# Optimization experiments

Measured on AMD Instinct MI355X. Metric: run time of the kernel, lower is better.

## Reference

```python
import jax, jax.numpy as jnp
import numpy as np

B, T, D = 64, 1024, 512
H, O = 512, 128
HALF = D // 2
ALPHA_M = 0.8


def setup_inputs() -> dict:
    key = jax.random.key(0)
    ks = jax.random.split(key, 6)
    s_in = 1.0 / np.sqrt(HALF)
    s_h = 1.0 / np.sqrt(H)
    return {
        "x": jax.random.normal(ks[0], (B, T, D), dtype=jnp.float32),
        "w1": jax.random.uniform(ks[1], (H, HALF), jnp.float32, -s_in, s_in),
        "b1": jnp.zeros((H,), jnp.float32),
        "tau1": jnp.full((H,), 3.0, jnp.float32),
        "w2": jax.random.uniform(ks[2], (H, HALF), jnp.float32, -s_in, s_in),
        "b2": jnp.zeros((H,), jnp.float32),
        "tau2": jnp.full((H,), 0.5, jnp.float32),
        "wo": jax.random.uniform(ks[3], (O, H), jnp.float32, -s_h, s_h),
        "bo": jnp.zeros((O,), jnp.float32),
    }


def reference(x, w1, b1, tau1, w2, b2, tau2, wo, bo):
    # Hoist the per-timestep branch Linears into two batched GEMMs.
    d1_in = jnp.einsum("bti,hi->tbh", x[:, :, :HALF], w1) + b1  # [T,B,H]
    d2_in = jnp.einsum("bti,hi->tbh", x[:, :, HALF:], w2) + b2  # [T,B,H]

    a1 = jax.nn.sigmoid(tau1)  # [H]
    a2 = jax.nn.sigmoid(tau2)  # [H]

    def step(carry, ins):
        d1, d2, mem = carry
        i1, i2 = ins
        d1 = a1 * d1 + (1.0 - a1) * i1
        d2 = a2 * d2 + (1.0 - a2) * i2
        mem = ALPHA_M * mem + (1.0 - ALPHA_M) * (d1 + d2)
        return (d1, d2, mem), mem

    z = jnp.zeros((x.shape[0], tau1.shape[0]), x.dtype)
    _, mems = jax.lax.scan(step, (z, z, z), (d1_in, d2_in))  # mems: [T,B,H]

    # Output projection + sigmoid, vectorized over all timesteps.
    out = jax.nn.sigmoid(jnp.einsum("tbh,oh->bto", mems, wo) + bo)  # [B,T,O]
    return out
```

## Files before the change

### kernel.cpp

```cpp
#include <hip/hip_runtime.h>


#define B_    64
#define T_    1024
#define D_    512
#define H_    512
#define O_    128
#define HALF_ 256
#define CLEN  32
#define NC    32

typedef __attribute__((ext_vector_type(4))) float        f32x4;
typedef __attribute__((ext_vector_type(2))) float        f32x2;
typedef __attribute__((ext_vector_type(8))) short        s16x8;
typedef __attribute__((ext_vector_type(4))) unsigned int u32x4;
typedef __attribute__((ext_vector_type(2))) unsigned int u32x2;

__device__ __forceinline__ unsigned short f2bf(float f) {
    unsigned u = __float_as_uint(f);
    return (unsigned short)((u + 0x7fffu + ((u >> 16) & 1u)) >> 16);
}
__device__ __forceinline__ unsigned packbf(float a, float b) {
    return (unsigned)f2bf(a) | ((unsigned)f2bf(b) << 16);
}
__device__ __forceinline__ float bflo(unsigned u) { return __uint_as_float(u << 16); }
__device__ __forceinline__ float bfhi(unsigned u) { return __uint_as_float(u & 0xffff0000u); }
__device__ __forceinline__ float sigf(float x) { return 1.f / (1.f + __expf(-x)); }
__device__ __forceinline__ float guard(float dn) {
    if (fabsf(dn) < 1e-6f) dn = (dn < 0.f ? -1e-6f : 1e-6f);
    return dn;
}
__device__ __forceinline__ float pw32(float a) {
    float t = a * a; t *= t; t *= t; t *= t; t *= t; return t;
}

typedef const __attribute__((address_space(1))) unsigned int gu32;
typedef __attribute__((address_space(3))) unsigned int      lu32;
__device__ __forceinline__ void gl_lds16(const void* g, void* l) {
    __builtin_amdgcn_global_load_lds((gu32*)g, (lu32*)l, 16, 0, 0);
}

__global__ __launch_bounds__(256) void gtab_kernel(
    const float* __restrict__ tau1, const float* __restrict__ tau2,
    float* __restrict__ G1, float* __restrict__ G2)
{
    const int h = blockIdx.x * 256 + threadIdx.x;
    const float a1 = sigf(tau1[h]), a2 = sigf(tau2[h]);
    const float c1 = 0.2f * a1 / guard(0.8f - a1);
    const float c2 = 0.2f * a2 / guard(0.8f - a2);
    float pm = 1.f, p1 = 1.f, p2 = 1.f;
    for (int k = 0; k < CLEN; ++k) {
        pm *= 0.8f; p1 *= a1; p2 *= a2;
        G1[k * H_ + h] = c1 * (pm - p1);
        G2[k * H_ + h] = c2 * (pm - p2);
    }
}

__global__ __launch_bounds__(256) void wcast_kernel(
    const float* __restrict__ w1, const float* __restrict__ w2,
    const float* __restrict__ wo,
    unsigned int* __restrict__ w1b, unsigned int* __restrict__ w2b,
    unsigned int* __restrict__ wob)
{
    const float* s; unsigned int* d; int n;
    if (blockIdx.y == 0)      { s = w1; d = w1b; n = H_ * HALF_; }
    else if (blockIdx.y == 1) { s = w2; d = w2b; n = H_ * HALF_; }
    else                      { s = wo; d = wob; n = O_ * H_;    }
    int i = (blockIdx.x * 256 + threadIdx.x) * 4;
    if (i >= n) return;
    f32x4 a = *(const f32x4*)(s + i);
    u32x2 p;
    p.x = packbf(a.x, a.y);
    p.y = packbf(a.z, a.w);
    *(u32x2*)(d + i / 2) = p;
}

__global__ __launch_bounds__(256) void cast_kernel(const float* __restrict__ x,
                                                   unsigned int* __restrict__ xb) {
    size_t i = ((size_t)blockIdx.x * 256 + threadIdx.x) * 8;
    f32x4 a = *(const f32x4*)(x + i);
    f32x4 b = *(const f32x4*)(x + i + 4);
    u32x4 p;
    p.x = packbf(a.x, a.y); p.y = packbf(a.z, a.w);
    p.z = packbf(b.x, b.y); p.w = packbf(b.z, b.w);
    *(u32x4*)(xb + i / 2) = p;
}

__global__ __launch_bounds__(256, 2) void gemm1f_kernel(
    const unsigned short* __restrict__ xb,
    const unsigned short* __restrict__ w1b, const unsigned short* __restrict__ w2b,
    const float* __restrict__ b1, const float* __restrict__ tau1,
    const float* __restrict__ b2, const float* __restrict__ tau2,
    unsigned int* __restrict__ mems,
    float* __restrict__ Sd1, float* __restrict__ Sd2, float* __restrict__ Sm)
{
    __shared__ short smem[32768];
    short* As1 = smem;
    short* As2 = smem + 8192;
    short* Bs1 = smem + 16384;
    short* Bs2 = smem + 24576;
    short* d1L = smem;
    short* d2L = smem + 16384;

    const int nt = blockIdx.x;
    const int mt = blockIdx.y;
    const int b  = mt >> 3;
    const int t0 = (mt & 7) << 7;

    const int tid = threadIdx.x, l = tid & 63, wv = tid >> 6;
    const int ln = l & 15, qd = l >> 4;
    const int wm = (wv & 1) << 6, wn = (wv >> 1) << 6;

    const unsigned short* abase  = xb + (size_t)(mt * 128) * D_;
    const unsigned short* w1base = w1b + (size_t)(nt * 128) * HALF_;
    const unsigned short* w2base = w2b + (size_t)(nt * 128) * HALF_;

    f32x4 acc0[4][4] = {};
    f32x4 acc1[4][4] = {};

    for (int kt = 0; kt < HALF_; kt += 64) {
        #pragma unroll
        for (int i = 0; i < 4; ++i) {
            int ch = wv * 4 + i;
            int r  = ch * 8 + (l >> 3);
            int kbl = (l & 7) ^ (r & 7);
            gl_lds16(abase + (size_t)r * D_ + kt + kbl * 8,         &As1[ch * 512 + l * 8]);
        }
        #pragma unroll
        for (int i = 0; i < 4; ++i) {
            int ch = wv * 4 + i;
            int r  = ch * 8 + (l >> 3);
            int kbl = (l & 7) ^ (r & 7);
            gl_lds16(abase + (size_t)r * D_ + HALF_ + kt + kbl * 8, &As2[ch * 512 + l * 8]);
        }
        #pragma unroll
        for (int i = 0; i < 4; ++i) {
            int ch = wv * 4 + i;
            int r  = ch * 8 + (l >> 3);
            int kbl = (l & 7) ^ (r & 7);
            gl_lds16(w1base + (size_t)r * HALF_ + kt + kbl * 8,     &Bs1[ch * 512 + l * 8]);
        }
        #pragma unroll
        for (int i = 0; i < 4; ++i) {
            int ch = wv * 4 + i;
            int r  = ch * 8 + (l >> 3);
            int kbl = (l & 7) ^ (r & 7);
            gl_lds16(w2base + (size_t)r * HALF_ + kt + kbl * 8,     &Bs2[ch * 512 + l * 8]);
        }
        __syncthreads();
        #pragma unroll
        for (int ks = 0; ks < 64; ks += 32) {
            s16x8 af[4], bfv[4];
            #pragma unroll
            for (int i = 0; i < 4; ++i) {
                int r = wm + i * 16 + ln;
                int kbp = ((ks >> 3) + qd) ^ (r & 7);
                af[i] = *(const s16x8*)&As1[r * 64 + kbp * 8];
            }
            #pragma unroll
            for (int j = 0; j < 4; ++j) {
                int r = wn + j * 16 + ln;
                int kbp = ((ks >> 3) + qd) ^ (r & 7);
                bfv[j] = *(const s16x8*)&Bs1[r * 64 + kbp * 8];
            }
            #pragma unroll
            for (int i = 0; i < 4; ++i)
                #pragma unroll
                for (int j = 0; j < 4; ++j)
                    acc0[i][j] = __builtin_amdgcn_mfma_f32_16x16x32_bf16(
                        af[i], bfv[j], acc0[i][j], 0, 0, 0);
            #pragma unroll
            for (int i = 0; i < 4; ++i) {
                int r = wm + i * 16 + ln;
                int kbp = ((ks >> 3) + qd) ^ (r & 7);
                af[i] = *(const s16x8*)&As2[r * 64 + kbp * 8];
            }
            #pragma unroll
            for (int j = 0; j < 4; ++j) {
                int r = wn + j * 16 + ln;
                int kbp = ((ks >> 3) + qd) ^ (r & 7);
                bfv[j] = *(const s16x8*)&Bs2[r * 64 + kbp * 8];
            }
            #pragma unroll
            for (int i = 0; i < 4; ++i)
                #pragma unroll
                for (int j = 0; j < 4; ++j)
                    acc1[i][j] = __builtin_amdgcn_mfma_f32_16x16x32_bf16(
                        af[i], bfv[j], acc1[i][j], 0, 0, 0);
        }
        __syncthreads();
    }

    #pragma unroll
    for (int i = 0; i < 4; ++i)
        #pragma unroll
        for (int j = 0; j < 4; ++j)
            #pragma unroll
            for (int r = 0; r < 4; ++r) {
                int t  = wm + i * 16 + qd * 4 + r;
                int hc = (wn + j * 16 + ln) ^ ((t & 12) << 2);
                d1L[t * 128 + hc] = (short)f2bf(acc0[i][j][r]);
                d2L[t * 128 + hc] = (short)f2bf(acc1[i][j][r]);
            }
    __syncthreads();

    const int cl  = tid >> 6;
    const int h2l = tid & 63;
    const int hl0 = h2l << 1;
    const int hg0 = nt * 128 + hl0;
    const int cg  = ((mt & 7) << 2) + cl;

    const float a1a = sigf(tau1[hg0]), a1b = sigf(tau1[hg0 + 1]);
    const float a2a = sigf(tau2[hg0]), a2b = sigf(tau2[hg0 + 1]);
    const float o1a = 1.f - a1a, o1b = 1.f - a1b;
    const float o2a = 1.f - a2a, o2b = 1.f - a2b;
    const float bb1a = b1[hg0], bb1b = b1[hg0 + 1];
    const float bb2a = b2[hg0], bb2b = b2[hg0 + 1];

    float d1a = 0.f, d1b = 0.f, d2a = 0.f, d2b = 0.f, ma = 0.f, mb = 0.f;
    const size_t mrow = (size_t)(b * T_ + t0 + cl * CLEN) * (H_ / 2) + nt * 64 + h2l;

    #pragma unroll 8
    for (int k = 0; k < CLEN; ++k) {
        int t  = cl * CLEN + k;
        int hc = hl0 ^ ((t & 12) << 2);
        unsigned u1 = *(const unsigned*)&d1L[t * 128 + hc];
        unsigned u2 = *(const unsigned*)&d2L[t * 128 + hc];
        float i1a = bflo(u1) + bb1a, i1b = bfhi(u1) + bb1b;
        float i2a = bflo(u2) + bb2a, i2b = bfhi(u2) + bb2b;
        d1a = a1a * d1a + o1a * i1a;  d1b = a1b * d1b + o1b * i1b;
        d2a = a2a * d2a + o2a * i2a;  d2b = a2b * d2b + o2b * i2b;
        ma = 0.8f * ma + 0.2f * (d1a + d2a);
        mb = 0.8f * mb + 0.2f * (d1b + d2b);
        mems[mrow + (size_t)k * (H_ / 2)] = packbf(ma, mb);
    }

    const size_t si = (size_t)(cg * B_ + b) * H_ + hg0;
    f32x2 v;
    v.x = d1a; v.y = d1b; *(f32x2*)&Sd1[si] = v;
    v.x = d2a; v.y = d2b; *(f32x2*)&Sd2[si] = v;
    v.x = ma;  v.y = mb;  *(f32x2*)&Sm[si]  = v;
}

__global__ __launch_bounds__(128) void scanB_kernel(
    const float* __restrict__ Sd1, const float* __restrict__ Sd2,
    const float* __restrict__ Sm,
    const float* __restrict__ tau1, const float* __restrict__ tau2,
    float* __restrict__ D1, float* __restrict__ D2, float* __restrict__ DM)
{
    const int g = blockIdx.x * 128 + threadIdx.x;
    const int h2 = g & 255, b = g >> 8, h0 = h2 << 1;

    const float a1a = sigf(tau1[h0]), a1b = sigf(tau1[h0 + 1]);
    const float a2a = sigf(tau2[h0]), a2b = sigf(tau2[h0 + 1]);
    const float amL = pw32(0.8f);
    const float a1La = pw32(a1a), a1Lb = pw32(a1b);
    const float a2La = pw32(a2a), a2Lb = pw32(a2b);

    const float c1a = 0.2f * a1a / guard(0.8f - a1a);
    const float c1b = 0.2f * a1b / guard(0.8f - a1b);
    const float c2a = 0.2f * a2a / guard(0.8f - a2a);
    const float c2b = 0.2f * a2b / guard(0.8f - a2b);

    const float g1La = c1a * (amL - a1La), g1Lb = c1b * (amL - a1Lb);
    const float g2La = c2a * (amL - a2La), g2Lb = c2b * (amL - a2Lb);

    float D1a = 0.f, D1b = 0.f, D2a = 0.f, D2b = 0.f, Ma = 0.f, Mb = 0.f;
    for (int c = 0; c < NC; ++c) {
        const size_t si = (size_t)(c * B_ + b) * H_ + h0;
        f32x2 v;
        v.x = D1a; v.y = D1b; *(f32x2*)&D1[si] = v;
        v.x = D2a; v.y = D2b; *(f32x2*)&D2[si] = v;
        v.x = Ma;  v.y = Mb;  *(f32x2*)&DM[si] = v;
        f32x2 s1 = *(const f32x2*)&Sd1[si];
        f32x2 s2 = *(const f32x2*)&Sd2[si];
        f32x2 sm = *(const f32x2*)&Sm[si];
        float nMa = amL * Ma + D1a * g1La + D2a * g2La + sm.x;
        float nMb = amL * Mb + D1b * g1Lb + D2b * g2Lb + sm.y;
        D1a = a1La * D1a + s1.x;  D1b = a1Lb * D1b + s1.y;
        D2a = a2La * D2a + s2.x;  D2b = a2Lb * D2b + s2.y;
        Ma = nMa;  Mb = nMb;
    }
}

__global__ __launch_bounds__(256, 2) void gemm2f_kernel(
    const unsigned short* __restrict__ mems, const unsigned short* __restrict__ wob,
    const float* __restrict__ bo,
    const float* __restrict__ G1, const float* __restrict__ G2,
    const float* __restrict__ D1, const float* __restrict__ D2,
    const float* __restrict__ DM, float* __restrict__ out)
{
    __shared__ short As[128 * 64];
    __shared__ short Bs[128 * 64];
    __shared__ float PMl[CLEN];

    const int mt = blockIdx.x;
    const int b = mt >> 3, c0 = (mt & 7) << 2;
    const int tid = threadIdx.x, l = tid & 63, wv = tid >> 6;
    const int ln = l & 15, qd = l >> 4;
    const int wm = (wv & 1) << 6, wn = (wv >> 1) << 6;

    if (tid < CLEN) {
        float pm = 1.f;
        for (int k = 0; k <= tid; ++k) pm *= 0.8f;
        PMl[tid] = pm;
    }
    __syncthreads();

    f32x4 acc[4][4] = {};
    const unsigned short* abase = mems + (size_t)(mt * 128) * H_;

    for (int kt = 0; kt < H_; kt += 64) {
        #pragma unroll
        for (int i = 0; i < 4; ++i) {
            int ch = wv * 4 + i;
            int r  = ch * 8 + (l >> 3);
            int kbl = (l & 7) ^ (r & 7);
            gl_lds16(wob + (size_t)r * H_ + kt + kbl * 8, &Bs[ch * 512 + l * 8]);
        }
        #pragma unroll
        for (int i = 0; i < 4; ++i) {
            int gi = i * 256 + tid;
            int r = gi >> 3, kbp = gi & 7, kbl = kbp ^ (r & 7);
            int h0 = kt + kbl * 8;
            int k = r & 31, c = c0 + (r >> 5);
            size_t dbase = (size_t)(c * B_ + b) * H_ + h0;
            f32x4 d1a = *(const f32x4*)&D1[dbase], d1b = *(const f32x4*)&D1[dbase + 4];
            f32x4 d2a = *(const f32x4*)&D2[dbase], d2b = *(const f32x4*)&D2[dbase + 4];
            f32x4 dma = *(const f32x4*)&DM[dbase], dmb = *(const f32x4*)&DM[dbase + 4];
            f32x4 g1a = *(const f32x4*)&G1[k * H_ + h0], g1b = *(const f32x4*)&G1[k * H_ + h0 + 4];
            f32x4 g2a = *(const f32x4*)&G2[k * H_ + h0], g2b = *(const f32x4*)&G2[k * H_ + h0 + 4];
            float pm = PMl[k];
            u32x4 mv = *(const u32x4*)(abase + (size_t)r * H_ + h0);
            float v0 = bflo(mv.x) + d1a.x * g1a.x + d2a.x * g2a.x + dma.x * pm;
            float v1 = bfhi(mv.x) + d1a.y * g1a.y + d2a.y * g2a.y + dma.y * pm;
            float v2 = bflo(mv.y) + d1a.z * g1a.z + d2a.z * g2a.z + dma.z * pm;
            float v3 = bfhi(mv.y) + d1a.w * g1a.w + d2a.w * g2a.w + dma.w * pm;
            float v4 = bflo(mv.z) + d1b.x * g1b.x + d2b.x * g2b.x + dmb.x * pm;
            float v5 = bfhi(mv.z) + d1b.y * g1b.y + d2b.y * g2b.y + dmb.y * pm;
            float v6 = bflo(mv.w) + d1b.z * g1b.z + d2b.z * g2b.z + dmb.z * pm;
            float v7 = bfhi(mv.w) + d1b.w * g1b.w + d2b.w * g2b.w + dmb.w * pm;
            u32x4 p;
            p.x = packbf(v0, v1); p.y = packbf(v2, v3);
            p.z = packbf(v4, v5); p.w = packbf(v6, v7);
            *(u32x4*)&As[r * 64 + kbp * 8] = p;
        }
        __syncthreads();
        #pragma unroll
        for (int ks = 0; ks < 64; ks += 32) {
            s16x8 af[4], bfv[4];
            #pragma unroll
            for (int i = 0; i < 4; ++i) {
                int r = wm + i * 16 + ln;
                int kbp = ((ks >> 3) + qd) ^ (r & 7);
                af[i] = *(const s16x8*)&As[r * 64 + kbp * 8];
            }
            #pragma unroll
            for (int j = 0; j < 4; ++j) {
                int r = wn + j * 16 + ln;
                int kbp = ((ks >> 3) + qd) ^ (r & 7);
                bfv[j] = *(const s16x8*)&Bs[r * 64 + kbp * 8];
            }
            #pragma unroll
            for (int i = 0; i < 4; ++i)
                #pragma unroll
                for (int j = 0; j < 4; ++j)
                    acc[i][j] = __builtin_amdgcn_mfma_f32_16x16x32_bf16(
                        af[i], bfv[j], acc[i][j], 0, 0, 0);
        }
        __syncthreads();
    }

    float bov[4];
    #pragma unroll
    for (int j = 0; j < 4; ++j) bov[j] = bo[wn + j * 16 + ln];

    float* orow = out + (size_t)(mt * 128 + wm + qd * 4) * O_ + wn + ln;
    #pragma unroll
    for (int i = 0; i < 4; ++i)
        #pragma unroll
        for (int j = 0; j < 4; ++j)
            #pragma unroll
            for (int r = 0; r < 4; ++r) {
                float v = acc[i][j][r] + bov[j];
                orow[(size_t)(i * 16 + r) * O_ + j * 16] = 1.f / (1.f + __expf(-v));
            }
}

extern "C" void kernel_launch(void* const* d_in, const int* in_sizes, int n_in,
                              void* d_out, int out_size, void* d_ws, size_t ws_size,
                              hipStream_t stream) {
    const float* x    = (const float*)d_in[0];
    const float* w1   = (const float*)d_in[1];
    const float* b1   = (const float*)d_in[2];
    const float* tau1 = (const float*)d_in[3];
    const float* w2   = (const float*)d_in[4];
    const float* b2   = (const float*)d_in[5];
    const float* tau2 = (const float*)d_in[6];
    const float* wo   = (const float*)d_in[7];
    const float* bo   = (const float*)d_in[8];
    float* out = (float*)d_out;

    char* w = (char*)d_ws;
    unsigned short* xb   = (unsigned short*)(w);
    unsigned int*   mems = (unsigned int*)(w + (size_t)64 * 1024 * 1024);
    float* Sd1 = (float*)(w + (size_t)128 * 1024 * 1024);
    float* Sd2 = Sd1 + (1u << 20);
    float* Sm  = Sd1 + (2u << 20);
    float* D1  = Sd1 + (3u << 20);
    float* D2  = Sd1 + (4u << 20);
    float* DM  = Sd1 + (5u << 20);
    float* G1  = Sd1 + (6u << 20);
    float* G2  = G1 + CLEN * H_;
    unsigned short* w1b = (unsigned short*)(G2 + CLEN * H_);
    unsigned short* w2b = w1b + (size_t)H_ * HALF_;
    unsigned short* wob = w2b + (size_t)H_ * HALF_;

    gtab_kernel<<<dim3(2), 256, 0, stream>>>(tau1, tau2, G1, G2);
    wcast_kernel<<<dim3(128, 3), 256, 0, stream>>>(w1, w2, wo,
                                                   (unsigned int*)w1b,
                                                   (unsigned int*)w2b,
                                                   (unsigned int*)wob);
    cast_kernel<<<dim3(16384), 256, 0, stream>>>(x, (unsigned int*)xb);
    gemm1f_kernel<<<dim3(4, 512), 256, 0, stream>>>(xb, w1b, w2b, b1, tau1, b2, tau2,
                                                    mems, Sd1, Sd2, Sm);
    scanB_kernel<<<dim3(128), 128, 0, stream>>>(Sd1, Sd2, Sm, tau1, tau2, D1, D2, DM);
    gemm2f_kernel<<<dim3(512), 256, 0, stream>>>((const unsigned short*)mems, wob, bo,
                                                 G1, G2, D1, D2, DM, out);
}
```

Baseline: 362.1 us.

## Double block size to 512 threads in both GEMM kernels, halving per-wave tiles

Both fused GEMM kernels now launch 8 waves per block instead of 4. Each wave owns a 64x32 output sub-tile, so it holds half as many accumulator registers and issues half the global-to-LDS loads. The in-block scan in gemm1f now gives each thread a single hidden column instead of a pair, using scalar bf16 loads and stores. The aim is more waves resident per CU for better latency hiding, at the cost of narrower (2-byte) memory accesses in the scan epilogue and a lower MFMA-to-LDS-read ratio per wave.

Measured after the change: 353.4 us. 1.02x faster.

```diff
diff --git a/kernel.cpp b/kernel.cpp
--- a/kernel.cpp
+++ b/kernel.cpp
@@ -24,6 +24,9 @@
     return (unsigned)f2bf(a) | ((unsigned)f2bf(b) << 16);
 }
 __device__ __forceinline__ float bflo(unsigned u) { return __uint_as_float(u << 16); }
+__device__ __forceinline__ float bfu16(unsigned short u) {
+    return __uint_as_float(((unsigned)u) << 16);
+}
 __device__ __forceinline__ float bfhi(unsigned u) { return __uint_as_float(u & 0xffff0000u); }
 __device__ __forceinline__ float sigf(float x) { return 1.f / (1.f + __expf(-x)); }
 __device__ __forceinline__ float guard(float dn) {
@@ -86,7 +89,7 @@
     *(u32x4*)(xb + i / 2) = p;
 }
 
-__global__ __launch_bounds__(256, 2) void gemm1f_kernel(
+__global__ __launch_bounds__(512, 4) void gemm1f_kernel(
     const unsigned short* __restrict__ xb,
     const unsigned short* __restrict__ w1b, const unsigned short* __restrict__ w2b,
     const float* __restrict__ b1, const float* __restrict__ tau1,
@@ -109,40 +112,41 @@
 
     const int tid = threadIdx.x, l = tid & 63, wv = tid >> 6;
     const int ln = l & 15, qd = l >> 4;
-    const int wm = (wv & 1) << 6, wn = (wv >> 1) << 6;
+    const int wm = (wv & 1) << 6;
+    const int wn = (wv >> 1) << 5;
 
     const unsigned short* abase  = xb + (size_t)(mt * 128) * D_;
     const unsigned short* w1base = w1b + (size_t)(nt * 128) * HALF_;
     const unsigned short* w2base = w2b + (size_t)(nt * 128) * HALF_;
 
-    f32x4 acc0[4][4] = {};
-    f32x4 acc1[4][4] = {};
+    f32x4 acc0[4][2] = {};
+    f32x4 acc1[4][2] = {};
 
     for (int kt = 0; kt < HALF_; kt += 64) {
         #pragma unroll
-        for (int i = 0; i < 4; ++i) {
-            int ch = wv * 4 + i;
+        for (int i = 0; i < 2; ++i) {
+            int ch = wv * 2 + i;
             int r  = ch * 8 + (l >> 3);
             int kbl = (l & 7) ^ (r & 7);
             gl_lds16(abase + (size_t)r * D_ + kt + kbl * 8,         &As1[ch * 512 + l * 8]);
         }
         #pragma unroll
-        for (int i = 0; i < 4; ++i) {
-            int ch = wv * 4 + i;
+        for (int i = 0; i < 2; ++i) {
+            int ch = wv * 2 + i;
             int r  = ch * 8 + (l >> 3);
             int kbl = (l & 7) ^ (r & 7);
             gl_lds16(abase + (size_t)r * D_ + HALF_ + kt + kbl * 8, &As2[ch * 512 + l * 8]);
         }
         #pragma unroll
-        for (int i = 0; i < 4; ++i) {
-            int ch = wv * 4 + i;
+        for (int i = 0; i < 2; ++i) {
+            int ch = wv * 2 + i;
             int r  = ch * 8 + (l >> 3);
             int kbl = (l & 7) ^ (r & 7);
             gl_lds16(w1base + (size_t)r * HALF_ + kt + kbl * 8,     &Bs1[ch * 512 + l * 8]);
         }
         #pragma unroll
-        for (int i = 0; i < 4; ++i) {
-            int ch = wv * 4 + i;
+        for (int i = 0; i < 2; ++i) {
+            int ch = wv * 2 + i;
             int r  = ch * 8 + (l >> 3);
             int kbl = (l & 7) ^ (r & 7);
             gl_lds16(w2base + (size_t)r * HALF_ + kt + kbl * 8,     &Bs2[ch * 512 + l * 8]);
@@ -150,7 +154,7 @@
         __syncthreads();
         #pragma unroll
         for (int ks = 0; ks < 64; ks += 32) {
-            s16x8 af[4], bfv[4];
+            s16x8 af[4], bfv[2];
             #pragma unroll
             for (int i = 0; i < 4; ++i) {
                 int r = wm + i * 16 + ln;
@@ -158,7 +162,7 @@
                 af[i] = *(const s16x8*)&As1[r * 64 + kbp * 8];
             }
             #pragma unroll
-            for (int j = 0; j < 4; ++j) {
+            for (int j = 0; j < 2; ++j) {
                 int r = wn + j * 16 + ln;
                 int kbp = ((ks >> 3) + qd) ^ (r & 7);
                 bfv[j] = *(const s16x8*)&Bs1[r * 64 + kbp * 8];
@@ -166,7 +170,7 @@
             #pragma unroll
             for (int i = 0; i < 4; ++i)
                 #pragma unroll
-                for (int j = 0; j < 4; ++j)
+                for (int j = 0; j < 2; ++j)
                     acc0[i][j] = __builtin_amdgcn_mfma_f32_16x16x32_bf16(
                         af[i], bfv[j], acc0[i][j], 0, 0, 0);
             #pragma unroll
@@ -176,7 +180,7 @@
                 af[i] = *(const s16x8*)&As2[r * 64 + kbp * 8];
             }
             #pragma unroll
-            for (int j = 0; j < 4; ++j) {
+            for (int j = 0; j < 2; ++j) {
                 int r = wn + j * 16 + ln;
                 int kbp = ((ks >> 3) + qd) ^ (r & 7);
                 bfv[j] = *(const s16x8*)&Bs2[r * 64 + kbp * 8];
@@ -184,7 +188,7 @@
             #pragma unroll
             for (int i = 0; i < 4; ++i)
                 #pragma unroll
-                for (int j = 0; j < 4; ++j)
+                for (int j = 0; j < 2; ++j)
                     acc1[i][j] = __builtin_amdgcn_mfma_f32_16x16x32_bf16(
                         af[i], bfv[j], acc1[i][j], 0, 0, 0);
         }
@@ -194,7 +198,7 @@
     #pragma unroll
     for (int i = 0; i < 4; ++i)
         #pragma unroll
-        for (int j = 0; j < 4; ++j)
+        for (int j = 0; j < 2; ++j)
             #pragma unroll
             for (int r = 0; r < 4; ++r) {
                 int t  = wm + i * 16 + qd * 4 + r;
@@ -204,42 +208,36 @@
             }
     __syncthreads();
 
-    const int cl  = tid >> 6;
-    const int h2l = tid & 63;
-    const int hl0 = h2l << 1;
-    const int hg0 = nt * 128 + hl0;
-    const int cg  = ((mt & 7) << 2) + cl;
-
-    const float a1a = sigf(tau1[hg0]), a1b = sigf(tau1[hg0 + 1]);
-    const float a2a = sigf(tau2[hg0]), a2b = sigf(tau2[hg0 + 1]);
-    const float o1a = 1.f - a1a, o1b = 1.f - a1b;
-    const float o2a = 1.f - a2a, o2b = 1.f - a2b;
-    const float bb1a = b1[hg0], bb1b = b1[hg0 + 1];
-    const float bb2a = b2[hg0], bb2b = b2[hg0 + 1];
-
-    float d1a = 0.f, d1b = 0.f, d2a = 0.f, d2b = 0.f, ma = 0.f, mb = 0.f;
-    const size_t mrow = (size_t)(b * T_ + t0 + cl * CLEN) * (H_ / 2) + nt * 64 + h2l;
+    const int cl = tid >> 7;
+    const int h  = tid & 127;
+    const int hg = nt * 128 + h;
+    const int cg = ((mt & 7) << 2) + cl;
+
+    const float a1 = sigf(tau1[hg]);
+    const float a2 = sigf(tau2[hg]);
+    const float o1 = 1.f - a1, o2 = 1.f - a2;
+    const float bb1 = b1[hg], bb2 = b2[hg];
+
+    float d1 = 0.f, d2 = 0.f, m = 0.f;
+    unsigned short* msh = (unsigned short*)mems;
+    const size_t mrow = (size_t)(b * T_ + t0 + cl * CLEN) * H_ + hg;
 
     #pragma unroll 8
     for (int k = 0; k < CLEN; ++k) {
         int t  = cl * CLEN + k;
-        int hc = hl0 ^ ((t & 12) << 2);
-        unsigned u1 = *(const unsigned*)&d1L[t * 128 + hc];
-        unsigned u2 = *(const unsigned*)&d2L[t * 128 + hc];
-        float i1a = bflo(u1) + bb1a, i1b = bfhi(u1) + bb1b;
-        float i2a = bflo(u2) + bb2a, i2b = bfhi(u2) + bb2b;
-        d1a = a1a * d1a + o1a * i1a;  d1b = a1b * d1b + o1b * i1b;
-        d2a = a2a * d2a + o2a * i2a;  d2b = a2b * d2b + o2b * i2b;
-        ma = 0.8f * ma + 0.2f * (d1a + d2a);
-        mb = 0.8f * mb + 0.2f * (d1b + d2b);
-        mems[mrow + (size_t)k * (H_ / 2)] = packbf(ma, mb);
-    }
-
-    const size_t si = (size_t)(cg * B_ + b) * H_ + hg0;
-    f32x2 v;
-    v.x = d1a; v.y = d1b; *(f32x2*)&Sd1[si] = v;
-    v.x = d2a; v.y = d2b; *(f32x2*)&Sd2[si] = v;
-    v.x = ma;  v.y = mb;  *(f32x2*)&Sm[si]  = v;
+        int hc = h ^ ((t & 12) << 2);
+        float i1 = bfu16((unsigned short)d1L[t * 128 + hc]) + bb1;
+        float i2 = bfu16((unsigned short)d2L[t * 128 + hc]) + bb2;
+        d1 = a1 * d1 + o1 * i1;
+        d2 = a2 * d2 + o2 * i2;
+        m  = 0.8f * m + 0.2f * (d1 + d2);
+        msh[mrow + (size_t)k * H_] = f2bf(m);
+    }
+
+    const size_t si = (size_t)(cg * B_ + b) * H_ + hg;
+    Sd1[si] = d1;
+    Sd2[si] = d2;
+    Sm[si]  = m;
 }
 
 __global__ __launch_bounds__(128) void scanB_kernel(
@@ -283,7 +281,7 @@
     }
 }
 
-__global__ __launch_bounds__(256, 2) void gemm2f_kernel(
+__global__ __launch_bounds__(512, 4) void gemm2f_kernel(
     const unsigned short* __restrict__ mems, const unsigned short* __restrict__ wob,
     const float* __restrict__ bo,
     const float* __restrict__ G1, const float* __restrict__ G2,
@@ -298,7 +296,8 @@
     const int b = mt >> 3, c0 = (mt & 7) << 2;
     const int tid = threadIdx.x, l = tid & 63, wv = tid >> 6;
     const int ln = l & 15, qd = l >> 4;
-    const int wm = (wv & 1) << 6, wn = (wv >> 1) << 6;
+    const int wm = (wv & 1) << 6;
+    const int wn = (wv >> 1) << 5;
 
     if (tid < CLEN) {
         float pm = 1.f;
@@ -307,20 +306,20 @@
     }
     __syncthreads();
 
-    f32x4 acc[4][4] = {};
+    f32x4 acc[4][2] = {};
     const unsigned short* abase = mems + (size_t)(mt * 128) * H_;
 
     for (int kt = 0; kt < H_; kt += 64) {
         #pragma unroll
-        for (int i = 0; i < 4; ++i) {
-            int ch = wv * 4 + i;
+        for (int i = 0; i < 2; ++i) {
+            int ch = wv * 2 + i;
             int r  = ch * 8 + (l >> 3);
             int kbl = (l & 7) ^ (r & 7);
             gl_lds16(wob + (size_t)r * H_ + kt + kbl * 8, &Bs[ch * 512 + l * 8]);
         }
         #pragma unroll
-        for (int i = 0; i < 4; ++i) {
-            int gi = i * 256 + tid;
+        for (int i = 0; i < 2; ++i) {
+            int gi = i * 512 + tid;
             int r = gi >> 3, kbp = gi & 7, kbl = kbp ^ (r & 7);
             int h0 = kt + kbl * 8;
             int k = r & 31, c = c0 + (r >> 5);
@@ -348,7 +347,7 @@
         __syncthreads();
         #pragma unroll
         for (int ks = 0; ks < 64; ks += 32) {
-            s16x8 af[4], bfv[4];
+            s16x8 af[4], bfv[2];
             #pragma unroll
             for (int i = 0; i < 4; ++i) {
                 int r = wm + i * 16 + ln;
@@ -356,7 +355,7 @@
                 af[i] = *(const s16x8*)&As[r * 64 + kbp * 8];
             }
             #pragma unroll
-            for (int j = 0; j < 4; ++j) {
+            for (int j = 0; j < 2; ++j) {
                 int r = wn + j * 16 + ln;
                 int kbp = ((ks >> 3) + qd) ^ (r & 7);
                 bfv[j] = *(const s16x8*)&Bs[r * 64 + kbp * 8];
@@ -364,22 +363,22 @@
             #pragma unroll
             for (int i = 0; i < 4; ++i)
                 #pragma unroll
-                for (int j = 0; j < 4; ++j)
+                for (int j = 0; j < 2; ++j)
                     acc[i][j] = __builtin_amdgcn_mfma_f32_16x16x32_bf16(
                         af[i], bfv[j], acc[i][j], 0, 0, 0);
         }
         __syncthreads();
     }
 
-    float bov[4];
+    float bov[2];
     #pragma unroll
-    for (int j = 0; j < 4; ++j) bov[j] = bo[wn + j * 16 + ln];
+    for (int j = 0; j < 2; ++j) bov[j] = bo[wn + j * 16 + ln];
 
     float* orow = out + (size_t)(mt * 128 + wm + qd * 4) * O_ + wn + ln;
     #pragma unroll
     for (int i = 0; i < 4; ++i)
         #pragma unroll
-        for (int j = 0; j < 4; ++j)
+        for (int j = 0; j < 2; ++j)
             #pragma unroll
             for (int r = 0; r < 4; ++r) {
                 float v = acc[i][j][r] + bov[j];
@@ -422,9 +421,9 @@
                                                    (unsigned int*)w2b,
                                                    (unsigned int*)wob);
     cast_kernel<<<dim3(16384), 256, 0, stream>>>(x, (unsigned int*)xb);
-    gemm1f_kernel<<<dim3(4, 512), 256, 0, stream>>>(xb, w1b, w2b, b1, tau1, b2, tau2,
+    gemm1f_kernel<<<dim3(4, 512), 512, 0, stream>>>(xb, w1b, w2b, b1, tau1, b2, tau2,
                                                     mems, Sd1, Sd2, Sm);
     scanB_kernel<<<dim3(128), 128, 0, stream>>>(Sd1, Sd2, Sm, tau1, tau2, D1, D2, DM);
-    gemm2f_kernel<<<dim3(512), 256, 0, stream>>>((const unsigned short*)mems, wob, bo,
+    gemm2f_kernel<<<dim3(512), 512, 0, stream>>>((const unsigned short*)mems, wob, bo,
                                                  G1, G2, D1, D2, DM, out);
 }
```
